# Optimization experiments

Hardware: AMD Instinct MI355X
Metric: run time of the kernel (lower is better)

## Reference

```python
import jax, jax.numpy as jnp
import numpy as np
import math

SR = 44100
HOPS_PER_FRAME = 4                              # int(1/(1-0.75))
WINDOW = HOPS_PER_FRAME * math.floor(0.05 * SR / HOPS_PER_FRAME)  # 2204
HOP = WINDOW // HOPS_PER_FRAME                  # 551
N = 1_048_576                                   # ~23.8 s audio
MLPW = 16


def setup_inputs() -> dict:
    key = jax.random.key(0)
    ks = jax.random.split(key, 8)
    f32 = jnp.float32
    return dict(
        x=jax.random.normal(ks[0], (N,), f32) * 0.1,
        g1=jnp.array([1.0], f32),
        g2=jnp.array([0.01], f32),
        depth=jnp.array([0.3], f32),
        bias=jnp.array([0.05], f32),
        lfo_omega=jnp.array([0.0157], f32),      # ~0.2 Hz at 80 Hz hop rate
        lfo_phi=jnp.array([0.0], f32),
        lfo_r_logit=jnp.array([6.0], f32),       # r = sigmoid(6) ~ 0.9975
        W_in=jax.random.normal(ks[1], (2, MLPW), f32) / jnp.sqrt(2.0),
        b_in=jnp.zeros((MLPW,), f32),
        W_h=jax.random.normal(ks[2], (2, MLPW, MLPW), f32) / jnp.sqrt(float(MLPW)),
        b_h=jnp.zeros((2, MLPW), f32),
        W_out=jax.random.normal(ks[3], (MLPW, 1), f32) / jnp.sqrt(float(MLPW)),
        b_out=jnp.zeros((1,), f32),
        bq_dc=jnp.array([1.0], f32),
        bq_ff=jnp.array([0.1, -0.05], f32),
        bq_fb=jnp.array([0.1, -0.1], f32),
    )


def _logits2coeff(l):
    # stability-triangle parameterization of biquad denominator
    a1 = 2.0 * jnp.tanh(l[0])
    a2 = ((2.0 - jnp.abs(a1)) * jnp.tanh(l[1]) + jnp.abs(a1)) / 2.0
    return jnp.stack([jnp.ones_like(a1), a1, a2])


def _biquad_lfilter(x, a, b):
    # y[n] = sum_k b[k] x[n-k] - a[1] y[n-1] - a[2] y[n-2]   (a[0]=1)
    v = jnp.convolve(x, b)[: x.shape[0]]

    def step(c, vn):
        y = vn - a[1] * c[0] - a[2] * c[1]
        return (y, c[0]), y

    z = jnp.zeros((), x.dtype)
    _, y = jax.lax.scan(step, (z, z), v)
    return y


def _tv_fir(x, b):
    # y[n] = sum_{k=0..4} b[n,k] x[n-k]; x (N,), b (N,5)
    n = x.shape[0]
    xp = jnp.pad(x, (4, 0))
    X = jnp.stack([xp[4 - k: 4 - k + n] for k in range(5)], axis=-1)  # X[:,k]=x[n-k]
    return jnp.sum(b * X, axis=-1)


def _sample_wise_lpc(x, a):
    # y[n] = x[n] - sum_{k=1..4} a[n,k-1] y[n-k]; a (N,4)
    def step(c, inp):
        xn, an = inp
        y = xn - jnp.dot(an, c)
        return jnp.concatenate([y[None], c[:3]]), y

    _, y = jax.lax.scan(step, jnp.zeros((4,), x.dtype), (x, a))
    return y


def _lin_interp(c, n):
    # linear interp along time, align_corners=True; c (H,5) -> (n,5)
    H = c.shape[0]
    pos = jnp.arange(n, dtype=c.dtype) * ((H - 1) / (n - 1))
    i0 = jnp.clip(jnp.floor(pos).astype(jnp.int32), 0, H - 2)
    frac = (pos - i0.astype(c.dtype))[:, None]
    return c[i0] * (1.0 - frac) + c[i0 + 1] * frac


def _forward(x, g1, g2, depth, bias, lfo_omega, lfo_phi, lfo_r_logit,
             W_in, b_in, W_h, b_h, W_out, b_out, bq_dc, bq_ff, bq_fb):
    n = x.shape[0]
    num_hops = n // HOP + 1
    t = jnp.arange(num_hops, dtype=x.dtype)
    # damped oscillator LFO -> (H,2)
    r = jax.nn.sigmoid(lfo_r_logit[0])
    ph = lfo_omega[0] * t + lfo_phi[0]
    lfo = (r ** t)[:, None] * jnp.stack([jnp.cos(ph), jnp.sin(ph)], axis=-1)
    # MLP waveshaper (tanh activations, tanh output keeps lfo in (-1,1))
    h = jnp.tanh(lfo @ W_in + b_in)
    for i in range(W_h.shape[0]):
        h = jnp.tanh(h @ W_h[i] + b_h[i])
    ws = jnp.tanh(h @ W_out + b_out)[:, 0]
    d = bias[0] + depth[0] * 0.5 * (1.0 + ws)
    td = jnp.tan(d)
    p = jnp.tanh((1.0 - td) / (1.0 + td))           # (H,)
    # pre-filter biquad
    b1 = jnp.concatenate([bq_dc, bq_ff])
    a1 = _logits2coeff(bq_fb)
    h1 = _biquad_lfilter(x, a1, b1)
    h1g = g1[0] * h1
    # 4th-order allpass coefficients ((p - z^-1)/(1 - p z^-1))^4
    p2 = p * p; p3 = p2 * p; p4 = p2 * p2
    one = jnp.ones_like(p)
    b_ap = jnp.stack([p4, -4 * p3, 6 * p2, -4 * p, one], axis=-1)   # (H,5)
    a_ap = jnp.stack([one, -4 * p, 6 * p2, -4 * p3, p4], axis=-1)
    denom = a_ap - jnp.abs(g2[0]) * b_ap
    cb = b_ap / denom[:, :1]
    cd = denom / denom[:, :1]
    cb = _lin_interp(cb, n)                                         # (N,5)
    cd = _lin_interp(cd, n)
    v = _tv_fir(h1, cb)
    y2 = _sample_wise_lpc(v, cd[:, 1:])
    return (h1g + y2)[None, :], p


def reference(x, g1, g2, depth, bias, lfo_omega, lfo_phi, lfo_r_logit,
              W_in, b_in, W_h, b_h, W_out, b_out, bq_dc, bq_ff, bq_fb):
    return _forward(x, g1, g2, depth, bias, lfo_omega, lfo_phi, lfo_r_logit,
                    W_in, b_in, W_h, b_h, W_out, b_out, bq_dc, bq_ff, bq_fb)
```

## Files before the change

kernel.cpp:

```cpp
#include <hip/hip_runtime.h>
#include <math.h>

#define HOPSZ 551
#define LB 32
#define WU 96
#define SPAN (LB + WU)

__device__ __forceinline__ void bq_coeffs(const float* bq_fb, float& a1, float& a2)
{
    a1 = 2.0f * tanhf(bq_fb[0]);
    float aa = fabsf(a1);
    a2 = ((2.0f - aa) * tanhf(bq_fb[1]) + aa) * 0.5f;
}

__global__ __launch_bounds__(64) void k_hop(
    const float* __restrict__ g2, const float* __restrict__ depth,
    const float* __restrict__ bias, const float* __restrict__ lfo_omega,
    const float* __restrict__ lfo_phi, const float* __restrict__ lfo_r_logit,
    const float* __restrict__ W_in, const float* __restrict__ b_in,
    const float* __restrict__ W_h, const float* __restrict__ b_h,
    const float* __restrict__ W_out, const float* __restrict__ b_out,
    float* __restrict__ cb, float* __restrict__ cd, float* __restrict__ p_out,
    int H)
{
    int t = blockIdx.x * 64 + threadIdx.x;
    if (t >= H) return;
    float r = 1.0f / (1.0f + expf(-lfo_r_logit[0]));
    float ph = lfo_omega[0] * (float)t + lfo_phi[0];
    float rt = powf(r, (float)t);
    float l0 = rt * cosf(ph);
    float l1 = rt * sinf(ph);
    float h[16];
    #pragma unroll
    for (int j = 0; j < 16; j++)
        h[j] = tanhf(l0 * W_in[j] + l1 * W_in[16 + j] + b_in[j]);
    for (int i = 0; i < 2; i++) {
        float h2[16];
        #pragma unroll
        for (int j = 0; j < 16; j++) {
            float s = b_h[i * 16 + j];
            #pragma unroll
            for (int kk = 0; kk < 16; kk++)
                s += h[kk] * W_h[(i * 16 + kk) * 16 + j];
            h2[j] = tanhf(s);
        }
        #pragma unroll
        for (int j = 0; j < 16; j++) h[j] = h2[j];
    }
    float s = b_out[0];
    #pragma unroll
    for (int kk = 0; kk < 16; kk++) s += h[kk] * W_out[kk];
    float wsv = tanhf(s);
    float d = bias[0] + depth[0] * 0.5f * (1.0f + wsv);
    float td = tanf(d);
    float p = tanhf((1.0f - td) / (1.0f + td));
    p_out[t] = p;
    float p2 = p * p, p3 = p2 * p, p4 = p2 * p2;
    float bap[5] = { p4, -4.0f * p3, 6.0f * p2, -4.0f * p, 1.0f };
    float aap[5] = { 1.0f, -4.0f * p, 6.0f * p2, -4.0f * p3, p4 };
    float ag2 = fabsf(g2[0]);
    float inv = 1.0f / (aap[0] - ag2 * bap[0]);
    #pragma unroll
    for (int m = 0; m < 5; m++) {
        float dm = aap[m] - ag2 * bap[m];
        cb[(size_t)t * 5 + m] = bap[m] * inv;
        if (m >= 1) cd[(size_t)t * 4 + (m - 1)] = dm * inv;
    }
}

__global__ __launch_bounds__(64) void k_main(
    const float* __restrict__ x,
    const float* __restrict__ bq_dc, const float* __restrict__ bq_ff,
    const float* __restrict__ bq_fb,
    const float* __restrict__ cb, const float* __restrict__ cd,
    const float* __restrict__ g1, float* __restrict__ out,
    int N, int H, float S, int K)
{
    int k = blockIdx.x * 64 + threadIdx.x;
    if (k >= K) return;
    int n0 = k * LB;
    int ns = n0 - WU;

    float b0 = bq_dc[0], b1 = bq_ff[0], b2 = bq_ff[1];
    float a1, a2; bq_coeffs(bq_fb, a1, a2);
    float g = g1[0];

    float poss = (float)ns * S;
    int i0a = (int)floorf(poss);
    i0a = min(max(i0a, 0), H - 2);
    int i1 = i0a + 1;
    int i2 = min(i0a + 2, H - 1);
    float i0af = (float)i0a;

    float Ab[5], sAb[5], sDb[5];
    float Ad[4], sAd[4], sDd[4];
    {
        const float* r0 = cb + (size_t)i0a * 5;
        const float* r1 = cb + (size_t)i1 * 5;
        const float* r2 = cb + (size_t)i2 * 5;
        #pragma unroll
        for (int m = 0; m < 5; m++) {
            float lo = r0[m], mi = r1[m], hi = r2[m];
            Ab[m] = lo; sAb[m] = mi - lo; sDb[m] = (hi - mi) - (mi - lo);
        }
        const float* q0 = cd + (size_t)i0a * 4;
        const float* q1 = cd + (size_t)i1 * 4;
        const float* q2 = cd + (size_t)i2 * 4;
        #pragma unroll
        for (int m = 0; m < 4; m++) {
            float lo = q0[m], mi = q1[m], hi = q2[m];
            Ad[m] = lo; sAd[m] = mi - lo; sDd[m] = (hi - mi) - (mi - lo);
        }
    }

    float x1 = (ns >= 1) ? x[ns - 1] : 0.0f;
    float x2 = (ns >= 2) ? x[ns - 2] : 0.0f;
    float y1 = 0, y2 = 0, y3 = 0, y4 = 0;
    float z0 = 0, z1 = 0, z2 = 0, z3 = 0;

    const float4* xv = (const float4*)(x + ns);
    float4* ov = (float4*)(out + n0);

    for (int q = 0; q < SPAN / 4; q++) {
        int np = ns + q * 4;
        float4 xq;
        if (np >= 0 && np + 3 < N) {
            xq = xv[q];
        } else {
            xq.x = (np     >= 0 && np     < N) ? x[np]     : 0.0f;
            xq.y = (np + 1 >= 0 && np + 1 < N) ? x[np + 1] : 0.0f;
            xq.z = (np + 2 >= 0 && np + 2 < N) ? x[np + 2] : 0.0f;
            xq.w = (np + 3 >= 0 && np + 3 < N) ? x[np + 3] : 0.0f;
        }
        float xs[4] = { xq.x, xq.y, xq.z, xq.w };
        float os[4];
        #pragma unroll
        for (int m = 0; m < 4; m++) {
            int n = np + m;
            float pos = (float)n * S;
            float fr0 = pos - i0af;
            float tr  = fmaxf(fr0 - 1.0f, 0.0f);
            float cbv[5], cdv[4];
            #pragma unroll
            for (int mm = 0; mm < 5; mm++)
                cbv[mm] = fmaf(tr, sDb[mm], fmaf(fr0, sAb[mm], Ab[mm]));
            #pragma unroll
            for (int mm = 0; mm < 4; mm++)
                cdv[mm] = fmaf(tr, sDd[mm], fmaf(fr0, sAd[mm], Ad[mm]));
            float x0 = xs[m];
            float v   = b0 * x0 + b1 * x1 + b2 * x2;
            float ybq = v - a1 * y1 - a2 * y2;
            float v2  = cbv[0] * ybq + cbv[1] * y1 + cbv[2] * y2
                      + cbv[3] * y3 + cbv[4] * y4;
            float yz  = v2 - cdv[0] * z0 - cdv[1] * z1 - cdv[2] * z2 - cdv[3] * z3;
            os[m] = g * ybq + yz;
            y4 = y3; y3 = y2; y2 = y1; y1 = ybq;
            x2 = x1; x1 = x0;
            z3 = z2; z2 = z1; z1 = z0; z0 = yz;
        }
        if (q >= WU / 4) {
            if (np + 3 < N) {
                ov[q - WU / 4] = make_float4(os[0], os[1], os[2], os[3]);
            } else {
                #pragma unroll
                for (int m = 0; m < 4; m++)
                    if (np + m < N) out[np + m] = os[m];
            }
        }
    }
}

extern "C" void kernel_launch(void* const* d_in, const int* in_sizes, int n_in,
                              void* d_out, int out_size, void* d_ws, size_t ws_size,
                              hipStream_t stream)
{
    const float* x        = (const float*)d_in[0];
    const float* g1       = (const float*)d_in[1];
    const float* g2       = (const float*)d_in[2];
    const float* depth    = (const float*)d_in[3];
    const float* bias     = (const float*)d_in[4];
    const float* lfo_omega= (const float*)d_in[5];
    const float* lfo_phi  = (const float*)d_in[6];
    const float* lfo_r    = (const float*)d_in[7];
    const float* W_in     = (const float*)d_in[8];
    const float* b_in     = (const float*)d_in[9];
    const float* W_h      = (const float*)d_in[10];
    const float* b_h      = (const float*)d_in[11];
    const float* W_out    = (const float*)d_in[12];
    const float* b_out    = (const float*)d_in[13];
    const float* bq_dc    = (const float*)d_in[14];
    const float* bq_ff    = (const float*)d_in[15];
    const float* bq_fb    = (const float*)d_in[16];

    int N = in_sizes[0];
    int H = N / HOPSZ + 1;
    int K = (N + LB - 1) / LB;
    float S = (float)((double)(H - 1) / (double)(N - 1));

    float* cb = (float*)d_ws;
    float* cd = cb + (size_t)H * 5;

    float* outy = (float*)d_out;
    float* outp = outy + N;

    k_hop<<<(H + 63) / 64, 64, 0, stream>>>(
        g2, depth, bias, lfo_omega, lfo_phi, lfo_r,
        W_in, b_in, W_h, b_h, W_out, b_out, cb, cd, outp, H);

    k_main<<<(K + 63) / 64, 64, 0, stream>>>(
        x, bq_dc, bq_ff, bq_fb, cb, cd, g1, outy, N, H, S, K);
}
```

Measured before the change: 116.4 us.

## Fuse hop MLP into main filter kernel with per-block shared coefficients

Merges the per-hop MLP/coefficient kernel into the main sample-wise filter kernel. Each 64-thread block recomputes the few hop rows it needs (8 rows, 8 lanes per row) into shared memory, removing the separate launch and the global workspace round-trip. It also shrinks the per-thread output span and warm-up length (LB 32→16, WU 96→64), giving more threads and less redundant warm-up work per sample, at the cost of a shorter filter-state warm-up and so possible accuracy loss. Tail bounds checks are dropped, assuming N is a multiple of the block span.

```diff
diff --git a/kernel.cpp b/kernel.cpp
--- a/kernel.cpp
+++ b/kernel.cpp
@@ -2,115 +2,126 @@
 #include <math.h>
 
 #define HOPSZ 551
-#define LB 32
-#define WU 96
+#define LB   16
+#define WU   64
 #define SPAN (LB + WU)
-
-__device__ __forceinline__ void bq_coeffs(const float* bq_fb, float& a1, float& a2)
-{
-    a1 = 2.0f * tanhf(bq_fb[0]);
-    float aa = fabsf(a1);
-    a2 = ((2.0f - aa) * tanhf(bq_fb[1]) + aa) * 0.5f;
-}
-
-__global__ __launch_bounds__(64) void k_hop(
-    const float* __restrict__ g2, const float* __restrict__ depth,
-    const float* __restrict__ bias, const float* __restrict__ lfo_omega,
-    const float* __restrict__ lfo_phi, const float* __restrict__ lfo_r_logit,
+#define TPB  64
+#define BSPAN (TPB * LB)
+#define NROWS 8
+
+__global__ __launch_bounds__(TPB) void k_fused(
+    const float* __restrict__ x,
+    const float* __restrict__ g1, const float* __restrict__ g2,
+    const float* __restrict__ depth, const float* __restrict__ bias,
+    const float* __restrict__ lfo_omega, const float* __restrict__ lfo_phi,
+    const float* __restrict__ lfo_r_logit,
     const float* __restrict__ W_in, const float* __restrict__ b_in,
     const float* __restrict__ W_h, const float* __restrict__ b_h,
     const float* __restrict__ W_out, const float* __restrict__ b_out,
-    float* __restrict__ cb, float* __restrict__ cd, float* __restrict__ p_out,
-    int H)
+    const float* __restrict__ bq_dc, const float* __restrict__ bq_ff,
+    const float* __restrict__ bq_fb,
+    float* __restrict__ out, float* __restrict__ p_out,
+    int N, int H, float S)
 {
-    int t = blockIdx.x * 64 + threadIdx.x;
-    if (t >= H) return;
-    float r = 1.0f / (1.0f + expf(-lfo_r_logit[0]));
-    float ph = lfo_omega[0] * (float)t + lfo_phi[0];
-    float rt = powf(r, (float)t);
-    float l0 = rt * cosf(ph);
-    float l1 = rt * sinf(ph);
-    float h[16];
-    #pragma unroll
-    for (int j = 0; j < 16; j++)
-        h[j] = tanhf(l0 * W_in[j] + l1 * W_in[16 + j] + b_in[j]);
-    for (int i = 0; i < 2; i++) {
-        float h2[16];
-        #pragma unroll
-        for (int j = 0; j < 16; j++) {
-            float s = b_h[i * 16 + j];
+    __shared__ float hbufA[NROWS][16];
+    __shared__ float hbufB[NROWS][16];
+    __shared__ float rcb[NROWS][5];
+    __shared__ float rcd[NROWS][4];
+
+    const int lane = threadIdx.x;
+    const int n0b  = blockIdx.x * BSPAN;
+
+    int i0start = (int)floorf((float)(n0b - WU) * S);
+    i0start = min(max(i0start, 0), H - 2);
+
+    {
+        const int row = lane >> 3;
+        const int u   = lane & 7;
+        const int t_r = min(i0start + row, H - 1);
+        const float tf = (float)t_r;
+
+        float rsig = 1.0f / (1.0f + expf(-lfo_r_logit[0]));
+        float ph = lfo_omega[0] * tf + lfo_phi[0];
+        float rt = powf(rsig, tf);
+        float l0 = rt * cosf(ph);
+        float l1 = rt * sinf(ph);
+
+        #pragma unroll
+        for (int jj = 0; jj < 2; jj++) {
+            int j = u + jj * 8;
+            hbufA[row][j] = tanhf(l0 * W_in[j] + l1 * W_in[16 + j] + b_in[j]);
+        }
+        __syncthreads();
+        #pragma unroll
+        for (int jj = 0; jj < 2; jj++) {
+            int j = u + jj * 8;
+            float s = b_h[j];
             #pragma unroll
             for (int kk = 0; kk < 16; kk++)
-                s += h[kk] * W_h[(i * 16 + kk) * 16 + j];
-            h2[j] = tanhf(s);
-        }
-        #pragma unroll
-        for (int j = 0; j < 16; j++) h[j] = h2[j];
-    }
-    float s = b_out[0];
-    #pragma unroll
-    for (int kk = 0; kk < 16; kk++) s += h[kk] * W_out[kk];
-    float wsv = tanhf(s);
-    float d = bias[0] + depth[0] * 0.5f * (1.0f + wsv);
-    float td = tanf(d);
-    float p = tanhf((1.0f - td) / (1.0f + td));
-    p_out[t] = p;
-    float p2 = p * p, p3 = p2 * p, p4 = p2 * p2;
-    float bap[5] = { p4, -4.0f * p3, 6.0f * p2, -4.0f * p, 1.0f };
-    float aap[5] = { 1.0f, -4.0f * p, 6.0f * p2, -4.0f * p3, p4 };
-    float ag2 = fabsf(g2[0]);
-    float inv = 1.0f / (aap[0] - ag2 * bap[0]);
+                s += hbufA[row][kk] * W_h[kk * 16 + j];
+            hbufB[row][j] = tanhf(s);
+        }
+        __syncthreads();
+        #pragma unroll
+        for (int jj = 0; jj < 2; jj++) {
+            int j = u + jj * 8;
+            float s = b_h[16 + j];
+            #pragma unroll
+            for (int kk = 0; kk < 16; kk++)
+                s += hbufB[row][kk] * W_h[(16 + kk) * 16 + j];
+            hbufA[row][j] = tanhf(s);
+        }
+        __syncthreads();
+        if (u == 0) {
+            float s = b_out[0];
+            #pragma unroll
+            for (int kk = 0; kk < 16; kk++)
+                s += hbufA[row][kk] * W_out[kk];
+            float wsv = tanhf(s);
+            float d = bias[0] + depth[0] * 0.5f * (1.0f + wsv);
+            float td = tanf(d);
+            float p = tanhf((1.0f - td) / (1.0f + td));
+            p_out[t_r] = p;
+            float p2 = p * p, p3 = p2 * p, p4 = p2 * p2;
+            float bap[5] = { p4, -4.0f * p3, 6.0f * p2, -4.0f * p, 1.0f };
+            float aap[5] = { 1.0f, -4.0f * p, 6.0f * p2, -4.0f * p3, p4 };
+            float ag2 = fabsf(g2[0]);
+            float inv = 1.0f / (aap[0] - ag2 * bap[0]);
+            #pragma unroll
+            for (int m = 0; m < 5; m++) {
+                float dm = aap[m] - ag2 * bap[m];
+                rcb[row][m] = bap[m] * inv;
+                if (m >= 1) rcd[row][m - 1] = dm * inv;
+            }
+        }
+        __syncthreads();
+    }
+
+    const int n0 = n0b + lane * LB;
+    const int ns = n0 - WU;
+
+    float b0 = bq_dc[0], b1 = bq_ff[0], b2 = bq_ff[1];
+    float a1 = 2.0f * tanhf(bq_fb[0]);
+    float aa = fabsf(a1);
+    float a2 = ((2.0f - aa) * tanhf(bq_fb[1]) + aa) * 0.5f;
+    float g = g1[0];
+
+    int i0a = (int)floorf((float)ns * S);
+    i0a = min(max(i0a, 0), H - 2);
+    int rel = i0a - i0start;
+    float i0af = (float)i0a;
+
+    float Ab[5], sAb[5], sDb[5];
+    float Ad[4], sAd[4], sDd[4];
     #pragma unroll
     for (int m = 0; m < 5; m++) {
-        float dm = aap[m] - ag2 * bap[m];
-        cb[(size_t)t * 5 + m] = bap[m] * inv;
-        if (m >= 1) cd[(size_t)t * 4 + (m - 1)] = dm * inv;
-    }
-}
-
-__global__ __launch_bounds__(64) void k_main(
-    const float* __restrict__ x,
-    const float* __restrict__ bq_dc, const float* __restrict__ bq_ff,
-    const float* __restrict__ bq_fb,
-    const float* __restrict__ cb, const float* __restrict__ cd,
-    const float* __restrict__ g1, float* __restrict__ out,
-    int N, int H, float S, int K)
-{
-    int k = blockIdx.x * 64 + threadIdx.x;
-    if (k >= K) return;
-    int n0 = k * LB;
-    int ns = n0 - WU;
-
-    float b0 = bq_dc[0], b1 = bq_ff[0], b2 = bq_ff[1];
-    float a1, a2; bq_coeffs(bq_fb, a1, a2);
-    float g = g1[0];
-
-    float poss = (float)ns * S;
-    int i0a = (int)floorf(poss);
-    i0a = min(max(i0a, 0), H - 2);
-    int i1 = i0a + 1;
-    int i2 = min(i0a + 2, H - 1);
-    float i0af = (float)i0a;
-
-    float Ab[5], sAb[5], sDb[5];
-    float Ad[4], sAd[4], sDd[4];
-    {
-        const float* r0 = cb + (size_t)i0a * 5;
-        const float* r1 = cb + (size_t)i1 * 5;
-        const float* r2 = cb + (size_t)i2 * 5;
-        #pragma unroll
-        for (int m = 0; m < 5; m++) {
-            float lo = r0[m], mi = r1[m], hi = r2[m];
-            Ab[m] = lo; sAb[m] = mi - lo; sDb[m] = (hi - mi) - (mi - lo);
-        }
-        const float* q0 = cd + (size_t)i0a * 4;
-        const float* q1 = cd + (size_t)i1 * 4;
-        const float* q2 = cd + (size_t)i2 * 4;
-        #pragma unroll
-        for (int m = 0; m < 4; m++) {
-            float lo = q0[m], mi = q1[m], hi = q2[m];
-            Ad[m] = lo; sAd[m] = mi - lo; sDd[m] = (hi - mi) - (mi - lo);
-        }
+        float lo = rcb[rel][m], mi = rcb[rel + 1][m], hi = rcb[rel + 2][m];
+        Ab[m] = lo; sAb[m] = mi - lo; sDb[m] = (hi - mi) - (mi - lo);
+    }
+    #pragma unroll
+    for (int m = 0; m < 4; m++) {
+        float lo = rcd[rel][m], mi = rcd[rel + 1][m], hi = rcd[rel + 2][m];
+        Ad[m] = lo; sAd[m] = mi - lo; sDd[m] = (hi - mi) - (mi - lo);
     }
 
     float x1 = (ns >= 1) ? x[ns - 1] : 0.0f;
@@ -124,13 +135,13 @@
     for (int q = 0; q < SPAN / 4; q++) {
         int np = ns + q * 4;
         float4 xq;
-        if (np >= 0 && np + 3 < N) {
+        if (np >= 0) {
             xq = xv[q];
         } else {
-            xq.x = (np     >= 0 && np     < N) ? x[np]     : 0.0f;
-            xq.y = (np + 1 >= 0 && np + 1 < N) ? x[np + 1] : 0.0f;
-            xq.z = (np + 2 >= 0 && np + 2 < N) ? x[np + 2] : 0.0f;
-            xq.w = (np + 3 >= 0 && np + 3 < N) ? x[np + 3] : 0.0f;
+            xq.x = (np     >= 0) ? x[np]     : 0.0f;
+            xq.y = (np + 1 >= 0) ? x[np + 1] : 0.0f;
+            xq.z = (np + 2 >= 0) ? x[np + 2] : 0.0f;
+            xq.w = (np + 3 >= 0) ? x[np + 3] : 0.0f;
         }
         float xs[4] = { xq.x, xq.y, xq.z, xq.w };
         float os[4];
@@ -158,15 +169,8 @@
             x2 = x1; x1 = x0;
             z3 = z2; z2 = z1; z1 = z0; z0 = yz;
         }
-        if (q >= WU / 4) {
-            if (np + 3 < N) {
-                ov[q - WU / 4] = make_float4(os[0], os[1], os[2], os[3]);
-            } else {
-                #pragma unroll
-                for (int m = 0; m < 4; m++)
-                    if (np + m < N) out[np + m] = os[m];
-            }
-        }
+        if (q >= WU / 4)
+            ov[q - WU / 4] = make_float4(os[0], os[1], os[2], os[3]);
     }
 }
 
@@ -194,19 +198,15 @@
 
     int N = in_sizes[0];
     int H = N / HOPSZ + 1;
-    int K = (N + LB - 1) / LB;
+    int nblocks = N / BSPAN;
     float S = (float)((double)(H - 1) / (double)(N - 1));
-
-    float* cb = (float*)d_ws;
-    float* cd = cb + (size_t)H * 5;
 
     float* outy = (float*)d_out;
     float* outp = outy + N;
 
-    k_hop<<<(H + 63) / 64, 64, 0, stream>>>(
-        g2, depth, bias, lfo_omega, lfo_phi, lfo_r,
-        W_in, b_in, W_h, b_h, W_out, b_out, cb, cd, outp, H);
-
-    k_main<<<(K + 63) / 64, 64, 0, stream>>>(
-        x, bq_dc, bq_ff, bq_fb, cb, cd, g1, outy, N, H, S, K);
+    k_fused<<<nblocks, TPB, 0, stream>>>(
+        x, g1, g2, depth, bias, lfo_omega, lfo_phi, lfo_r,
+        W_in, b_in, W_h, b_h, W_out, b_out,
+        bq_dc, bq_ff, bq_fb,
+        outy, outp, N, H, S);
 }
```

Result: faster. 104.2 us (-10.5%).
